# Kernel tuning notes

Measured on AMD Instinct MI355X. Metric: run time of the kernel, lower is better.

The kernel has to match this reference:

```python
import jax, jax.numpy as jnp
import numpy as np

NUM_HEADS = 12
DIM = 768
HEAD_DIM = DIM // NUM_HEADS


def setup_inputs() -> dict:
    key = jax.random.key(0)
    ks = jax.random.split(key, 10)
    B, S = 4, 2048
    x = jax.random.normal(ks[0], (B, S, DIM), dtype=jnp.float32)
    attn_mask = jnp.zeros((B, S), dtype=jnp.float32)  # additive mask
    scale = 0.02
    Wq = jax.random.normal(ks[1], (DIM, DIM), dtype=jnp.float32) * scale
    bq = jnp.zeros((DIM,), dtype=jnp.float32)
    Wk = jax.random.normal(ks[2], (DIM, DIM), dtype=jnp.float32) * scale
    bk = jnp.zeros((DIM,), dtype=jnp.float32)
    Wv = jax.random.normal(ks[3], (DIM, DIM), dtype=jnp.float32) * scale
    bv = jnp.zeros((DIM,), dtype=jnp.float32)
    Wo = jax.random.normal(ks[4], (DIM, DIM), dtype=jnp.float32) * scale
    bo = jnp.zeros((DIM,), dtype=jnp.float32)
    return {"x": x, "attn_mask": attn_mask, "Wq": Wq, "bq": bq,
            "Wk": Wk, "bk": bk, "Wv": Wv, "bv": bv, "Wo": Wo, "bo": bo}


def reference(x, attn_mask, Wq, bq, Wk, bk, Wv, bv, Wo, bo):
    B, S, D = x.shape
    H, Hd = NUM_HEADS, HEAD_DIM
    scaling = Hd ** -0.5

    def split_heads(e):  # [B,S,D] -> [B,H,S,Hd]
        return e.reshape(B, S, H, Hd).transpose(0, 2, 1, 3)

    q = split_heads((x @ Wq + bq) * scaling)
    k = split_heads(x @ Wk + bk)
    v = split_heads(x @ Wv + bv)

    scores = jnp.einsum('bhqd,bhkd->bhqk', q, k)
    scores = scores + attn_mask[:, None, None, :]  # additive mask [B,1,1,S]
    probs = jax.nn.softmax(scores, axis=-1)
    out = jnp.einsum('bhqk,bhkd->bhqd', probs, v)  # [B,H,S,Hd]
    out = out.transpose(0, 2, 1, 3).reshape(B, S, D)
    return out @ Wo + bo
```

## Files before the change

### kernel.cpp

```cpp
#include <hip/hip_runtime.h>
#include <hip/hip_bf16.h>
#include <cstdint>
#include <cstddef>

#define DIM   768
#define NH    12
#define HD    64
#define BATCH 4
#define SEQ   2048
#define MTOT  (BATCH*SEQ)
#define NQKV  (3*DIM)

#define LOG2E 1.4426950408889634f

typedef __attribute__((ext_vector_type(8))) short bf16x8;
typedef __attribute__((ext_vector_type(4))) short bf16x4;
typedef __attribute__((ext_vector_type(4))) float f32x4;

__device__ __forceinline__ short f2bf(float f){
  union { __hip_bfloat16 h; short s; } u;
  u.h = __float2bfloat16(f);
  return u.s;
}

#if defined(__HIP_DEVICE_COMPILE__) && __has_builtin(__builtin_amdgcn_exp2f)
#define EXP2(x) __builtin_amdgcn_exp2f(x)
#else
#define EXP2(x) exp2f(x)
#endif

__device__ __forceinline__ f32x4 mfma32(bf16x8 a, bf16x8 b, f32x4 c){
  return __builtin_amdgcn_mfma_f32_16x16x32_bf16(a, b, c, 0, 0, 0);
}

__device__ __forceinline__ void gl_lds16(const short* g, short* l){
  __builtin_amdgcn_global_load_lds(
      (const __attribute__((address_space(1))) unsigned int*)g,
      (__attribute__((address_space(3))) unsigned int*)l,
      16, 0, 0);
}


__global__ __launch_bounds__(256) void pack_all(
    const float* __restrict__ x,
    const float* __restrict__ Wq, const float* __restrict__ Wk,
    const float* __restrict__ Wv, const float* __restrict__ Wo,
    const float* __restrict__ bq, const float* __restrict__ bk,
    const float* __restrict__ bv, const float* __restrict__ mask,
    short* __restrict__ xb, short* __restrict__ wqkv, short* __restrict__ wot,
    float* __restrict__ bqkv, float* __restrict__ mask2)
{
  const int NX = MTOT*DIM/4;
  const int NW = DIM*DIM;
  int gid = blockIdx.x * 256 + threadIdx.x;

  if (gid < NX){
    float4 v = ((const float4*)x)[gid];
    bf16x4 o;
    o[0] = f2bf(v.x); o[1] = f2bf(v.y); o[2] = f2bf(v.z); o[3] = f2bf(v.w);
    ((bf16x4*)xb)[gid] = o;
    return;
  }
  gid -= NX;
  if (gid < 4*NW){
    const int m = gid / NW;
    const int idx = gid - m*NW;
    const int n = idx / DIM, k = idx - n*DIM;
    const float* W = (m == 0) ? Wq : (m == 1) ? Wk : (m == 2) ? Wv : Wo;
    const short v = f2bf(W[k*DIM + n]);
    if (m < 3) wqkv[m*NW + idx] = v; else wot[idx] = v;
    return;
  }
  gid -= 4*NW;
  if (gid < NQKV)
    bqkv[gid] = (gid < DIM) ? bq[gid] : (gid < 2*DIM) ? bk[gid-DIM] : bv[gid-2*DIM];
  if (gid < BATCH*SEQ)
    mask2[gid] = mask[gid] * LOG2E;
}


template<int MODE>
__global__ __launch_bounds__(256, 3) void gemm_lds(
    const short* __restrict__ A,
    const short* __restrict__ Bt,
    const float* __restrict__ bias,
    short* __restrict__ o0, short* __restrict__ o1, short* __restrict__ o2,
    float* __restrict__ fo)
{
  __shared__ short ldsA[2][128*32];
  __shared__ short ldsB[2][128*32];

  const int tid = threadIdx.x;
  const int w  = tid >> 6, l = tid & 63;
  const int lr = l & 15,  lg = l >> 4;
  const int wr = w >> 1,  wc = w & 1;
  const int mBase = blockIdx.y * 128;
  const int nBase = blockIdx.x * 128;

  const int srow = w*16 + (l >> 2);
  const int scol = (l & 3) * 8;
  const short* gA = A  + (size_t)(mBase + srow) * DIM + scol;
  const short* gB = Bt + (size_t)(nBase + srow) * DIM + scol;

#define STAGE(BUF, KK) do {                                  \
    gl_lds16(gA + (KK),          &ldsA[BUF][w*512]);         \
    gl_lds16(gA + 64*DIM + (KK), &ldsA[BUF][2048 + w*512]);  \
    gl_lds16(gB + (KK),          &ldsB[BUF][w*512]);         \
    gl_lds16(gB + 64*DIM + (KK), &ldsB[BUF][2048 + w*512]);  \
  } while(0)

  f32x4 acc[4][4] = {};
  STAGE(0, 0);
  for (int kt = 0; kt < 24; ++kt){
    const int cur = kt & 1;
    __syncthreads();
    if (kt < 23){
      if (cur) STAGE(0, (kt+1)*32); else STAGE(1, (kt+1)*32);
    }
    bf16x8 a[4], b[4];
#pragma unroll
    for (int i = 0; i < 4; ++i){
      a[i] = *(const bf16x8*)&ldsA[cur][(wr*64 + i*16 + lr)*32 + lg*8];
      b[i] = *(const bf16x8*)&ldsB[cur][(wc*64 + i*16 + lr)*32 + lg*8];
    }
#pragma unroll
    for (int i = 0; i < 4; ++i)
#pragma unroll
      for (int j = 0; j < 4; ++j)
        acc[i][j] = mfma32(a[i], b[j], acc[i][j]);
  }
#undef STAGE

  if (MODE == 0){
    const int sect  = nBase / DIM;
    const int nloc0 = nBase - sect*DIM + wc*64;
    const float scl = (sect == 0) ? 0.125f*LOG2E : 1.0f;
#pragma unroll
    for (int j = 0; j < 4; ++j){
      const int nl = nloc0 + j*16 + lr;
      const int h = nl >> 6, d = nl & (HD-1);
      const float bn = bias[nBase + wc*64 + j*16 + lr];
#pragma unroll
      for (int i = 0; i < 4; ++i){
#pragma unroll
        for (int r = 0; r < 4; ++r){
          const int m = mBase + wr*64 + i*16 + lg*4 + r;
          const float val = (acc[i][j][r] + bn) * scl;
          const int b_ = m >> 11, s_ = m & (SEQ-1);
          const int bh = b_*NH + h;
          if (sect == 0){
            o0[((size_t)bh*SEQ + s_)*HD + d] = f2bf(val);
          } else if (sect == 1){
            const size_t idx = (((size_t)bh*64 + (s_>>5))*4
                                + ((s_>>4)&1)*2 + (d>>5))*512
                             + ((s_&15) + ((d>>3)&3)*16)*8 + (d&7);
            o1[idx] = f2bf(val);
          } else {
            const int p = (((s_>>2)&3)<<3) | (((s_>>4)&1)<<2) | (s_&3);
            const size_t idx = (((size_t)bh*64 + (s_>>5))*4 + (d>>4))*512
                             + ((d&15) + (p>>3)*16)*8 + (p&7);
            o2[idx] = f2bf(val);
          }
        }
      }
    }
  } else {
#pragma unroll
    for (int j = 0; j < 4; ++j){
      const int n = nBase + wc*64 + j*16 + lr;
      const float bn = bias[n];
#pragma unroll
      for (int i = 0; i < 4; ++i){
#pragma unroll
        for (int r = 0; r < 4; ++r){
          const int m = mBase + wr*64 + i*16 + lg*4 + r;
          fo[(size_t)m * DIM + n] = acc[i][j][r] + bn;
        }
      }
    }
  }
}


__global__ __launch_bounds__(256, 3) void attn_kernel(
    const short* __restrict__ q,
    const short* __restrict__ kimg,
    const short* __restrict__ vimg,
    const float* __restrict__ mask2,
    short* __restrict__ ao)
{
  __shared__ short ldsK[2][4096];
  __shared__ short ldsV[2][4096];

  const int tid = threadIdx.x;
  const int l = tid & 63, w = tid >> 6;
  const int lr = l & 15, lg = l >> 4;
  const int bh = blockIdx.x;
  const int b_ = bh / NH;
  const int h  = bh - b_*NH;
  const int qbase = blockIdx.y * 128 + w * 32;

  const short* qh   = q + (size_t)bh * SEQ * HD;
  const short* kSrc = kimg + (size_t)bh * 64 * 2048 + w*512 + l*8;
  const short* vSrc = vimg + (size_t)bh * 64 * 2048 + w*512 + l*8;
  const float* mRow = mask2 + (size_t)b_ * SEQ + lg*4;

  bf16x8 qf[2][2];
#pragma unroll
  for (int t = 0; t < 2; ++t){
    qf[t][0] = *(const bf16x8*)&qh[(size_t)(qbase + t*16 + lr)*HD + lg*8];
    qf[t][1] = *(const bf16x8*)&qh[(size_t)(qbase + t*16 + lr)*HD + 32 + lg*8];
  }

  bf16x8 ones;
#pragma unroll
  for (int j = 0; j < 8; ++j) ones[j] = (short)0x3F80;

  f32x4 o[2][4] = {};
  f32x4 lacc[2] = {};

#define ASTAGE(BUF, ST) do {                                          \
    gl_lds16(kSrc + (size_t)(ST)*4096,        &ldsK[BUF][w*512]);     \
    gl_lds16(kSrc + (size_t)(ST)*4096 + 2048, &ldsK[BUF][2048+w*512]);\
    gl_lds16(vSrc + (size_t)(ST)*4096,        &ldsV[BUF][w*512]);     \
    gl_lds16(vSrc + (size_t)(ST)*4096 + 2048, &ldsV[BUF][2048+w*512]);\
  } while(0)

  ASTAGE(0, 0);
  __syncthreads();

  for (int st = 0; st < 32; ++st){
    const int cur = st & 1;
    if (st < 31) ASTAGE(cur^1, st+1);

#pragma unroll
    for (int sub = 0; sub < 2; ++sub){
      bf16x8 kf[4], vf[4];
#pragma unroll
      for (int f = 0; f < 4; ++f){
        kf[f] = *(const bf16x8*)&ldsK[cur][sub*2048 + f*512 + l*8];
        vf[f] = *(const bf16x8*)&ldsV[cur][sub*2048 + f*512 + l*8];
      }
      const int koff = st*64 + sub*32;
      const float4 mv0 = *(const float4*)(mRow + koff);
      const float4 mv1 = *(const float4*)(mRow + koff + 16);

      bf16x8 pf[2];
#pragma unroll
      for (int t = 0; t < 2; ++t){
        f32x4 s0 = {}, s1 = {};
        s0 = mfma32(kf[0], qf[t][0], s0);
        s0 = mfma32(kf[1], qf[t][1], s0);
        s1 = mfma32(kf[2], qf[t][0], s1);
        s1 = mfma32(kf[3], qf[t][1], s1);
        const float p0 = EXP2(s0[0] + mv0.x);
        const float p1 = EXP2(s0[1] + mv0.y);
        const float p2 = EXP2(s0[2] + mv0.z);
        const float p3 = EXP2(s0[3] + mv0.w);
        const float p4 = EXP2(s1[0] + mv1.x);
        const float p5 = EXP2(s1[1] + mv1.y);
        const float p6 = EXP2(s1[2] + mv1.z);
        const float p7 = EXP2(s1[3] + mv1.w);
        pf[t][0]=f2bf(p0); pf[t][1]=f2bf(p1); pf[t][2]=f2bf(p2); pf[t][3]=f2bf(p3);
        pf[t][4]=f2bf(p4); pf[t][5]=f2bf(p5); pf[t][6]=f2bf(p6); pf[t][7]=f2bf(p7);
      }
      __builtin_amdgcn_s_setprio(1);
#pragma unroll
      for (int dblk = 0; dblk < 4; ++dblk){
        o[0][dblk] = mfma32(vf[dblk], pf[0], o[0][dblk]);
        o[1][dblk] = mfma32(vf[dblk], pf[1], o[1][dblk]);
      }
      lacc[0] = mfma32(ones, pf[0], lacc[0]);
      lacc[1] = mfma32(ones, pf[1], lacc[1]);
      __builtin_amdgcn_s_setprio(0);
    }
    __syncthreads();
  }
#undef ASTAGE

#pragma unroll
  for (int t = 0; t < 2; ++t){
    const float rinv = 1.f / lacc[t][0];
    const int qrow = qbase + t*16 + lr;
    const size_t rowbase = ((size_t)b_*SEQ + qrow) * DIM + h*HD;
#pragma unroll
    for (int dblk = 0; dblk < 4; ++dblk){
      bf16x4 ov;
#pragma unroll
      for (int r = 0; r < 4; ++r) ov[r] = f2bf(o[t][dblk][r] * rinv);
      *(bf16x4*)&ao[rowbase + dblk*16 + lg*4] = ov;
    }
  }
}


extern "C" void kernel_launch(void* const* d_in, const int* in_sizes, int n_in,
                              void* d_out, int out_size, void* d_ws, size_t ws_size,
                              hipStream_t stream) {
  const float* x    = (const float*)d_in[0];
  const float* mask = (const float*)d_in[1];
  const float* Wq   = (const float*)d_in[2];
  const float* bq   = (const float*)d_in[3];
  const float* Wk   = (const float*)d_in[4];
  const float* bk   = (const float*)d_in[5];
  const float* Wv   = (const float*)d_in[6];
  const float* bv   = (const float*)d_in[7];
  const float* Wo   = (const float*)d_in[8];
  const float* bo   = (const float*)d_in[9];
  float* out = (float*)d_out;

  char* ws = (char*)d_ws;
  const size_t SZ_XB = (size_t)MTOT * DIM * sizeof(short);
  const size_t SZ_W  = (size_t)DIM * DIM * sizeof(short);

  short* xb   = (short*)ws;            ws += SZ_XB;
  short* wqkv = (short*)ws;            ws += 3*SZ_W;
  short* wot  = (short*)ws;            ws += SZ_W;
  short* qb   = (short*)ws;            ws += SZ_XB;
  short* kimg = (short*)ws;            ws += SZ_XB;
  short* vimg = (short*)ws;            ws += SZ_XB;
  short* ao   = (short*)ws;            ws += SZ_XB;
  float* bqkv = (float*)ws;            ws += NQKV * sizeof(float);
  float* mask2= (float*)ws;            ws += (size_t)BATCH*SEQ*sizeof(float);

  const int NPACK = MTOT*DIM/4 + 4*DIM*DIM + BATCH*SEQ;
  pack_all<<<(NPACK + 255)/256, 256, 0, stream>>>(
      x, Wq, Wk, Wv, Wo, bq, bk, bv, mask, xb, wqkv, wot, bqkv, mask2);

  dim3 qkvgrid(NQKV/128, MTOT/128);
  gemm_lds<0><<<qkvgrid, 256, 0, stream>>>(xb, wqkv, bqkv, qb, kimg, vimg, nullptr);

  dim3 agrid(BATCH*NH, SEQ/128);
  attn_kernel<<<agrid, 256, 0, stream>>>(qb, kimg, vimg, mask2, ao);

  dim3 ogrid(DIM/128, MTOT/128);
  gemm_lds<1><<<ogrid, 256, 0, stream>>>(ao, wot, bo, nullptr, nullptr, nullptr, out);
}
```

Baseline: 160.2 us.

## Pre-tile GEMM operands into contiguous MFMA-ready image layout

The packing kernel, and the attention kernel's output writer, now store bf16 operands in a tiled 'image' layout in which each 128x32 k-slab is contiguous and already arranged in MFMA fragment order. The GEMM can then stage tiles with fully contiguous global-to-LDS loads and read fragments with linear LDS addressing, avoiding strided row loads and possible bank conflicts. The weight-pack step now reads float4s coalesced but scatters its writes, and the grid order is swapped so M tiles vary fastest.

```diff
diff --git a/kernel.cpp b/kernel.cpp
--- a/kernel.cpp
+++ b/kernel.cpp
@@ -38,6 +38,12 @@
       (const __attribute__((address_space(1))) unsigned int*)g,
       (__attribute__((address_space(3))) unsigned int*)l,
       16, 0, 0);
+}
+
+__device__ __forceinline__ size_t img_idx(int m, int k){
+  const int mt = m >> 7, r = m & 127, ks = k >> 5, c = k & 31;
+  return ((size_t)(mt*24 + ks))*4096 + (size_t)((r>>6)*2048 + ((r>>4)&3)*512
+       + ((r&15) + ((c>>3)<<4))*8 + (c&7));
 }
 
 
@@ -50,28 +56,36 @@
     short* __restrict__ xb, short* __restrict__ wqkv, short* __restrict__ wot,
     float* __restrict__ bqkv, float* __restrict__ mask2)
 {
-  const int NX = MTOT*DIM/4;
-  const int NW = DIM*DIM;
+  const int NX4 = MTOT*DIM/4;
+  const int NW4 = DIM*DIM/4;
   int gid = blockIdx.x * 256 + threadIdx.x;
 
-  if (gid < NX){
+  if (gid < NX4){
     float4 v = ((const float4*)x)[gid];
+    const int e = gid*4;
+    const int m = e / DIM, k = e - m*DIM;
     bf16x4 o;
     o[0] = f2bf(v.x); o[1] = f2bf(v.y); o[2] = f2bf(v.z); o[3] = f2bf(v.w);
-    ((bf16x4*)xb)[gid] = o;
+    *(bf16x4*)&xb[img_idx(m, k)] = o;
     return;
   }
-  gid -= NX;
-  if (gid < 4*NW){
-    const int m = gid / NW;
-    const int idx = gid - m*NW;
-    const int n = idx / DIM, k = idx - n*DIM;
-    const float* W = (m == 0) ? Wq : (m == 1) ? Wk : (m == 2) ? Wv : Wo;
-    const short v = f2bf(W[k*DIM + n]);
-    if (m < 3) wqkv[m*NW + idx] = v; else wot[idx] = v;
+  gid -= NX4;
+  if (gid < 4*NW4){
+    const int mat = gid / NW4;
+    const int rem = gid - mat*NW4;
+    const int e = rem*4;
+    const int k = e / DIM, n = e - k*DIM;
+    const float* W = (mat == 0) ? Wq : (mat == 1) ? Wk : (mat == 2) ? Wv : Wo;
+    const float4 v = *(const float4*)&W[e];
+    short* img = (mat < 3) ? wqkv : wot;
+    const int ng = (mat < 3) ? mat*DIM + n : n;
+    img[img_idx(ng+0, k)] = f2bf(v.x);
+    img[img_idx(ng+1, k)] = f2bf(v.y);
+    img[img_idx(ng+2, k)] = f2bf(v.z);
+    img[img_idx(ng+3, k)] = f2bf(v.w);
     return;
   }
-  gid -= 4*NW;
+  gid -= 4*NW4;
   if (gid < NQKV)
     bqkv[gid] = (gid < DIM) ? bq[gid] : (gid < 2*DIM) ? bk[gid-DIM] : bv[gid-2*DIM];
   if (gid < BATCH*SEQ)
@@ -81,32 +95,31 @@
 
 template<int MODE>
 __global__ __launch_bounds__(256, 3) void gemm_lds(
-    const short* __restrict__ A,
-    const short* __restrict__ Bt,
+    const short* __restrict__ Aimg,
+    const short* __restrict__ Bimg,
     const float* __restrict__ bias,
     short* __restrict__ o0, short* __restrict__ o1, short* __restrict__ o2,
     float* __restrict__ fo)
 {
-  __shared__ short ldsA[2][128*32];
-  __shared__ short ldsB[2][128*32];
+  __shared__ short ldsA[2][4096];
+  __shared__ short ldsB[2][4096];
 
   const int tid = threadIdx.x;
   const int w  = tid >> 6, l = tid & 63;
   const int lr = l & 15,  lg = l >> 4;
   const int wr = w >> 1,  wc = w & 1;
-  const int mBase = blockIdx.y * 128;
-  const int nBase = blockIdx.x * 128;
-
-  const int srow = w*16 + (l >> 2);
-  const int scol = (l & 3) * 8;
-  const short* gA = A  + (size_t)(mBase + srow) * DIM + scol;
-  const short* gB = Bt + (size_t)(nBase + srow) * DIM + scol;
-
-#define STAGE(BUF, KK) do {                                  \
-    gl_lds16(gA + (KK),          &ldsA[BUF][w*512]);         \
-    gl_lds16(gA + 64*DIM + (KK), &ldsA[BUF][2048 + w*512]);  \
-    gl_lds16(gB + (KK),          &ldsB[BUF][w*512]);         \
-    gl_lds16(gB + 64*DIM + (KK), &ldsB[BUF][2048 + w*512]);  \
+  const int mt = blockIdx.x, nt = blockIdx.y;
+  const int mBase = mt * 128;
+  const int nBase = nt * 128;
+
+  const short* gA = Aimg + (size_t)mt*24*4096 + w*512 + l*8;
+  const short* gB = Bimg + (size_t)nt*24*4096 + w*512 + l*8;
+
+#define STAGE(BUF, KS) do {                                     \
+    gl_lds16(gA + (KS)*4096,        &ldsA[BUF][w*512]);         \
+    gl_lds16(gA + (KS)*4096 + 2048, &ldsA[BUF][2048 + w*512]);  \
+    gl_lds16(gB + (KS)*4096,        &ldsB[BUF][w*512]);         \
+    gl_lds16(gB + (KS)*4096 + 2048, &ldsB[BUF][2048 + w*512]);  \
   } while(0)
 
   f32x4 acc[4][4] = {};
@@ -114,14 +127,12 @@
   for (int kt = 0; kt < 24; ++kt){
     const int cur = kt & 1;
     __syncthreads();
-    if (kt < 23){
-      if (cur) STAGE(0, (kt+1)*32); else STAGE(1, (kt+1)*32);
-    }
+    if (kt < 23) STAGE(cur^1, kt+1);
     bf16x8 a[4], b[4];
 #pragma unroll
     for (int i = 0; i < 4; ++i){
-      a[i] = *(const bf16x8*)&ldsA[cur][(wr*64 + i*16 + lr)*32 + lg*8];
-      b[i] = *(const bf16x8*)&ldsB[cur][(wc*64 + i*16 + lr)*32 + lg*8];
+      a[i] = *(const bf16x8*)&ldsA[cur][wr*2048 + i*512 + l*8];
+      b[i] = *(const bf16x8*)&ldsB[cur][wc*2048 + i*512 + l*8];
     }
 #pragma unroll
     for (int i = 0; i < 4; ++i)
@@ -281,14 +292,18 @@
 #pragma unroll
   for (int t = 0; t < 2; ++t){
     const float rinv = 1.f / lacc[t][0];
-    const int qrow = qbase + t*16 + lr;
-    const size_t rowbase = ((size_t)b_*SEQ + qrow) * DIM + h*HD;
+    const int m = b_*SEQ + qbase + t*16 + lr;
+    const int mt = m >> 7, r = m & 127;
+    short* abase = ao + (size_t)mt*24*4096
+                 + (r>>6)*2048 + ((r>>4)&3)*512;
 #pragma unroll
     for (int dblk = 0; dblk < 4; ++dblk){
       bf16x4 ov;
 #pragma unroll
-      for (int r = 0; r < 4; ++r) ov[r] = f2bf(o[t][dblk][r] * rinv);
-      *(bf16x4*)&ao[rowbase + dblk*16 + lg*4] = ov;
+      for (int rr = 0; rr < 4; ++rr) ov[rr] = f2bf(o[t][dblk][rr] * rinv);
+      const int k = h*64 + dblk*16 + lg*4;
+      const int ks = k >> 5, c = k & 31;
+      *(bf16x4*)&abase[(size_t)ks*4096 + ((r&15) + ((c>>3)<<4))*8 + (c&7)] = ov;
     }
   }
 }
@@ -323,16 +338,16 @@
   float* bqkv = (float*)ws;            ws += NQKV * sizeof(float);
   float* mask2= (float*)ws;            ws += (size_t)BATCH*SEQ*sizeof(float);
 
-  const int NPACK = MTOT*DIM/4 + 4*DIM*DIM + BATCH*SEQ;
+  const int NPACK = MTOT*DIM/4 + DIM*DIM + BATCH*SEQ;
   pack_all<<<(NPACK + 255)/256, 256, 0, stream>>>(
       x, Wq, Wk, Wv, Wo, bq, bk, bv, mask, xb, wqkv, wot, bqkv, mask2);
 
-  dim3 qkvgrid(NQKV/128, MTOT/128);
+  dim3 qkvgrid(MTOT/128, NQKV/128);
   gemm_lds<0><<<qkvgrid, 256, 0, stream>>>(xb, wqkv, bqkv, qb, kimg, vimg, nullptr);
 
   dim3 agrid(BATCH*NH, SEQ/128);
   attn_kernel<<<agrid, 256, 0, stream>>>(qb, kimg, vimg, mask2, ao);
 
-  dim3 ogrid(DIM/128, MTOT/128);
+  dim3 ogrid(MTOT/128, DIM/128);
   gemm_lds<1><<<ogrid, 256, 0, stream>>>(ao, wot, bo, nullptr, nullptr, nullptr, out);
 }
```

Measured after the change: 150.4 us. -6.2%, faster.
